# Kernel tuning notes

Measured on AMD Instinct MI355X. Metric: run time of the kernel, lower is better.

Reference implementation:

```python
import jax, jax.numpy as jnp
import numpy as np

B, P, ENC, DEC, ATT, EMB, V, MAXLEN = 64, 196, 2048, 1024, 1024, 1024, 10000, 20


def setup_inputs() -> dict:
    key = jax.random.key(0)
    ks = jax.random.split(key, 20)
    s = 0.02
    inp = {
        'encoder_out': jax.random.normal(ks[0], (B, 14, 14, ENC), jnp.float32),
        'encoded_captions': jax.random.randint(ks[1], (B, MAXLEN), 0, V),
        'caption_lengths': jax.random.randint(ks[2], (B, 1), 2, MAXLEN + 1).at[0, 0].set(MAXLEN),
        # embedding
        'emb_table': jax.random.uniform(ks[3], (V, EMB), jnp.float32, -0.1, 0.1),
        # attention MLP (weight_norm Linear == plain Linear math)
        'We': jax.random.normal(ks[4], (ATT, ENC)) * s,
        'be': jnp.zeros((ATT,), jnp.float32),
        'Wd': jax.random.normal(ks[5], (ATT, DEC)) * s,
        'bd': jnp.zeros((ATT,), jnp.float32),
        'Wf': jax.random.normal(ks[6], (1, ATT)) * s,
        'bf': jnp.zeros((1,), jnp.float32),
        # top_down_attention LSTMCell: input = EMB+ENC+DEC
        'W_ih1': jax.random.normal(ks[7], (4 * DEC, EMB + ENC + DEC)) * s,
        'W_hh1': jax.random.normal(ks[8], (4 * DEC, DEC)) * s,
        'b_ih1': jnp.zeros((4 * DEC,), jnp.float32),
        'b_hh1': jnp.zeros((4 * DEC,), jnp.float32),
        # language_model LSTMCell: input = ENC+DEC
        'W_ih2': jax.random.normal(ks[9], (4 * DEC, ENC + DEC)) * s,
        'W_hh2': jax.random.normal(ks[10], (4 * DEC, DEC)) * s,
        'b_ih2': jnp.zeros((4 * DEC,), jnp.float32),
        'b_hh2': jnp.zeros((4 * DEC,), jnp.float32),
        # output heads
        'Wfc1': jax.random.normal(ks[11], (V, DEC)) * s,
        'bfc1': jnp.zeros((V,), jnp.float32),
        'Wfc': jax.random.uniform(ks[12], (V, DEC), jnp.float32, -0.1, 0.1),
        'bfc': jnp.zeros((V,), jnp.float32),
    }
    return inp


def _lstm_cell(x, h, c, Wih, Whh, bih, bhh):
    g = x @ Wih.T + bih + h @ Whh.T + bhh
    i, f, gg, o = jnp.split(g, 4, axis=-1)  # torch gate order: i, f, g, o
    c2 = jax.nn.sigmoid(f) * c + jax.nn.sigmoid(i) * jnp.tanh(gg)
    h2 = jax.nn.sigmoid(o) * jnp.tanh(c2)
    return h2, c2


def _decode(encoder_out, encoded_captions, caption_lengths, emb_table,
            We, be, Wd, bd, Wf, bf,
            W_ih1, W_hh1, b_ih1, b_hh1, W_ih2, W_hh2, b_ih2, b_hh2,
            Wfc1, bfc1, Wfc, bfc):
    b = encoder_out.shape[0]
    enc = encoder_out.reshape(b, -1, encoder_out.shape[-1])  # (B,P,ENC)
    enc_mean = enc.mean(axis=1)
    cl = caption_lengths.squeeze(1)
    sort_ind = jnp.argsort(-cl)
    cl = cl[sort_ind]
    enc = enc[sort_ind]
    enc_mean = enc_mean[sort_ind]
    caps = encoded_captions[sort_ind]
    dec_len = cl - 1  # (B,)
    embeds = emb_table[caps]  # (B,T,EMB)
    Tdec = caps.shape[1] - 1
    # precompute encoder attention projection (loop-invariant, same math)
    att1 = jnp.einsum('bpe,ae->bpa', enc, We) + be  # (B,P,ATT)

    def step(carry, t):
        h1, c1, h2, c2 = carry
        active = (t < dec_len)[:, None]  # (B,1)
        x1 = jnp.concatenate([h2, enc_mean, embeds[:, t, :]], axis=1)
        h1n, c1n = _lstm_cell(x1, h1, c1, W_ih1, W_hh1, b_ih1, b_hh1)
        h1n = jnp.where(active, h1n, h1)
        c1n = jnp.where(active, c1n, c1)
        # Bahdanau attention
        att2 = h1n @ Wd.T + bd  # (B,ATT)
        e = jnp.einsum('bpa,a->bp', jax.nn.relu(att1 + att2[:, None, :]), Wf[0]) + bf[0]
        alpha = jax.nn.softmax(e, axis=1)
        awe = jnp.einsum('bpe,bp->be', enc, alpha)
        preds1 = h1n @ Wfc1.T + bfc1  # dropout is identity at eval
        x2 = jnp.concatenate([awe, h1n], axis=1)
        h2n, c2n = _lstm_cell(x2, h2, c2, W_ih2, W_hh2, b_ih2, b_hh2)
        h2n = jnp.where(active, h2n, h2)
        c2n = jnp.where(active, c2n, c2)
        preds = h2n @ Wfc.T + bfc
        preds = jnp.where(active, preds, 0.0)
        preds1 = jnp.where(active, preds1, 0.0)
        return (h1n, c1n, h2n, c2n), (preds, preds1)

    z = jnp.zeros((b, DEC), jnp.float32)
    (_, _, _, _), (pr, pr1) = jax.lax.scan(step, (z, z, z, z), jnp.arange(Tdec))
    predictions = jnp.transpose(pr, (1, 0, 2))  # (B,Tdec,V)
    predictions1 = jnp.transpose(pr1, (1, 0, 2))
    return predictions, predictions1, caps, dec_len, sort_ind


def reference(encoder_out, encoded_captions, caption_lengths, emb_table,
              We, be, Wd, bd, Wf, bf,
              W_ih1, W_hh1, b_ih1, b_hh1, W_ih2, W_hh2, b_ih2, b_hh2,
              Wfc1, bfc1, Wfc, bfc):
    return _decode(encoder_out, encoded_captions, caption_lengths, emb_table,
                   We, be, Wd, bd, Wf, bf,
                   W_ih1, W_hh1, b_ih1, b_hh1, W_ih2, W_hh2, b_ih2, b_hh2,
                   Wfc1, bfc1, Wfc, bfc)
```

## Files before the change

kernel.cpp:

```cpp
#include <hip/hip_runtime.h>
#include <cmath>

#define B_ 64
#define P_ 196
#define ENC_ 2048
#define DEC_ 1024
#define V_ 10000
#define MAXLEN_ 20
#define TDEC_ 19

typedef __attribute__((ext_vector_type(8))) short bf16x8;
typedef __attribute__((ext_vector_type(4))) float f32x4;


__device__ __align__(16) short g_encb[(size_t)12544 * 2048];
__device__ __align__(16) short g_encbt[(size_t)12544 * 2048];
__device__ __align__(16) short g_att1[(size_t)12544 * 1024];
__device__ __align__(16) short g_Wp1t[(size_t)4096 * 2048];
__device__ __align__(16) short g_Wmid1t[(size_t)4096 * 3072];
__device__ __align__(16) short g_Wc2t[(size_t)4096 * 4096];
__device__ __align__(16) short g_Webt[(size_t)1024 * 2048];
__device__ __align__(16) short g_Wdt[(size_t)1024 * 1024];
__device__ __align__(16) short g_Wfc1t[(size_t)10000 * 1024];
__device__ __align__(16) short g_Wfct[(size_t)10000 * 1024];
__device__ __align__(16) short g_xs1[(size_t)20 * 64 * 2048];
__device__ __align__(16) short g_xmid[(size_t)19 * 64 * 3072];
__device__ __align__(16) short g_xc2[(size_t)20 * 64 * 4096];
__device__ __align__(16) short g_em[64 * 2048];
__device__ __align__(16) float g_pre1[(size_t)19 * 64 * 4096];
__device__ __align__(16) float g_part[(size_t)8 * 64 * 4096];
__device__ __align__(16) float g_att2p[(size_t)4 * 64 * 1024];
__device__ __align__(16) float g_e[64 * P_];
__device__ __align__(16) float g_c1[64 * 1024];
__device__ __align__(16) float g_c2[64 * 1024];
__device__ int g_ibuf[64 + 64 + 64 * MAXLEN_];

__device__ __forceinline__ short f2b(float f) {
  unsigned u = __float_as_uint(f);
  u += 0x7FFFu + ((u >> 16) & 1u);
  return (short)(u >> 16);
}
__device__ __forceinline__ float b2f(short s) {
  return __uint_as_float(((unsigned)(unsigned short)s) << 16);
}

__global__ void k_sort(const int* __restrict__ cl_in, const int* __restrict__ caps_in,
                       int* __restrict__ sind, int* __restrict__ declen, int* __restrict__ caps_s,
                       float* __restrict__ out_caps, float* __restrict__ out_declen,
                       float* __restrict__ out_sind) {
  int i = threadIdx.x;
  __shared__ int cl[B_];
  cl[i] = cl_in[i];
  __syncthreads();
  int my = cl[i], pos = 0;
  for (int j = 0; j < B_; ++j) {
    int cj = cl[j];
    if (cj > my || (cj == my && j < i)) pos++;
  }
  sind[pos] = i;
  __syncthreads();
  int sb = sind[i];
  int dl = cl[sb] - 1;
  declen[i] = dl;
  out_declen[i] = (float)dl;
  out_sind[i] = (float)sb;
  for (int t = 0; t < MAXLEN_; ++t) {
    int v = caps_in[sb * MAXLEN_ + t];
    caps_s[i * MAXLEN_ + t] = v;
    out_caps[i * MAXLEN_ + t] = (float)v;
  }
}

__global__ __launch_bounds__(256) void k_encprep(const float* __restrict__ enc,
                                                 const int* __restrict__ sind,
                                                 short* __restrict__ encb,
                                                 short* __restrict__ encbt) {
  int mg = blockIdx.x;
  int b = mg / P_, p = mg - b * P_;
  int tid = threadIdx.x;
  const float* src = enc + ((size_t)sind[b] * P_ + p) * ENC_ + tid * 8;
  float4 a = *(const float4*)src;
  float4 c = *(const float4*)(src + 4);
  bf16x8 v;
  v[0] = f2b(a.x); v[1] = f2b(a.y); v[2] = f2b(a.z); v[3] = f2b(a.w);
  v[4] = f2b(c.x); v[5] = f2b(c.y); v[6] = f2b(c.z); v[7] = f2b(c.w);
  *(bf16x8*)(encb + (size_t)mg * ENC_ + tid * 8) = v;
  size_t off = (((size_t)(mg >> 4) * 64 + (tid >> 2)) << 9) +
               (((mg & 15) | ((tid & 3) << 4)) << 3);
  *(bf16x8*)(encbt + off) = v;
}

__global__ __launch_bounds__(256) void k_encmeanb(const short* __restrict__ encb,
                                                  short* __restrict__ em) {
  int b = blockIdx.x;
  int col0 = threadIdx.x * 8;
  const short* src = encb + (size_t)b * P_ * ENC_ + col0;
  float acc[8] = {};
  for (int p = 0; p < P_; ++p) {
    bf16x8 v = *(const bf16x8*)(src + (size_t)p * ENC_);
#pragma unroll
    for (int j = 0; j < 8; ++j) acc[j] += b2f(v[j]);
  }
#pragma unroll
  for (int j = 0; j < 8; ++j) em[b * 2048 + col0 + j] = f2b(acc[j] * (1.0f / 196.0f));
}

__global__ __launch_bounds__(256) void k_prefill(const float* __restrict__ emb,
                                                 const int* __restrict__ caps_s,
                                                 const short* __restrict__ em,
                                                 short* __restrict__ xmid) {
  int t = blockIdx.x, b = blockIdx.y, tid = threadIdx.x;
  short* xr = xmid + ((size_t)t * 64 + b) * 3072;
  int i = tid * 8;
  *(bf16x8*)(xr + i) = *(const bf16x8*)(em + b * 2048 + i);
  int cap = caps_s[b * MAXLEN_ + t];
  int j = tid * 4;
  float4 v = *(const float4*)(emb + (size_t)cap * 1024 + j);
  short4 o;
  o.x = f2b(v.x); o.y = f2b(v.y); o.z = f2b(v.z); o.w = f2b(v.w);
  *(short4*)(xr + 2048 + j) = o;
}

__global__ void k_f2bts(const float* __restrict__ src, int Kstride, int c0, int ncols,
                        short* __restrict__ dst, int Ktot, int koff) {
  int idx = blockIdx.x * 256 + threadIdx.x;
  int kc = ncols >> 3;
  int r = idx / kc, k8 = (idx - r * kc) << 3;
  const float* s = src + (size_t)r * Kstride + c0 + k8;
  float4 a = *(const float4*)s;
  float4 c = *(const float4*)(s + 4);
  bf16x8 v;
  v[0] = f2b(a.x); v[1] = f2b(a.y); v[2] = f2b(a.z); v[3] = f2b(a.w);
  v[4] = f2b(c.x); v[5] = f2b(c.y); v[6] = f2b(c.z); v[7] = f2b(c.w);
  int kg = koff + k8;
  size_t off = (((size_t)(r >> 4) * (Ktot >> 5) + (kg >> 5)) << 9) +
               (((r & 15) | (((kg >> 3) & 3) << 4)) << 3);
  *(bf16x8*)(dst + off) = v;
}

__global__ __launch_bounds__(1024) void k_att1_t(const short* __restrict__ At,
                                                 const short* __restrict__ Wt,
                                                 const float* __restrict__ be,
                                                 short* __restrict__ Cb) {
  int wave = threadIdx.x >> 6, lane = threadIdx.x & 63;
  int mt0 = blockIdx.x * 8 + (wave >> 3) * 4;
  int nt0 = blockIdx.y * 32 + (wave & 7) * 4;
  f32x4 acc[4][4] = {};
  const short* Ab = At + ((size_t)mt0 * 64 << 9) + lane * 8;
  const short* Wb = Wt + ((size_t)nt0 * 64 << 9) + lane * 8;
  for (int kt = 0; kt < 64; ++kt) {
    bf16x8 a[4], b[4];
#pragma unroll
    for (int i = 0; i < 4; ++i) a[i] = *(const bf16x8*)(Ab + (((size_t)i * 64 + kt) << 9));
#pragma unroll
    for (int j = 0; j < 4; ++j) b[j] = *(const bf16x8*)(Wb + (((size_t)j * 64 + kt) << 9));
#pragma unroll
    for (int i = 0; i < 4; ++i)
#pragma unroll
      for (int j = 0; j < 4; ++j)
        acc[i][j] = __builtin_amdgcn_mfma_f32_16x16x32_bf16(a[i], b[j], acc[i][j], 0, 0, 0);
  }
  int rr = (lane >> 4) * 4, cc = lane & 15;
  int m0 = mt0 * 16, n0 = nt0 * 16;
#pragma unroll
  for (int i = 0; i < 4; ++i)
#pragma unroll
    for (int j = 0; j < 4; ++j) {
      int n = n0 + j * 16 + cc;
      float bn = be[n];
#pragma unroll
      for (int r = 0; r < 4; ++r) {
        int m = m0 + i * 16 + rr + r;
        Cb[(size_t)m * 1024 + n] = f2b(acc[i][j][r] + bn);
      }
    }
}

__global__ __launch_bounds__(256) void k_skinny_t(const short* __restrict__ A, int lda,
                                                  const short* __restrict__ Wt, int ldw,
                                                  int N, int kchunk, float* __restrict__ part) {
  int wave = threadIdx.x >> 6, lane = threadIdx.x & 63;
  int n0 = blockIdx.x * 128 + wave * 32;
  int kb = blockIdx.y * kchunk;
  int lr = lane & 15, lk = (lane >> 4) * 8;
  int ntk = ldw >> 5;
  int nt0 = n0 >> 4;
  f32x4 acc[4][2] = {};
  const short* Ab = A + (size_t)lr * lda + kb + lk;
  const short* Wb0 = Wt + (((size_t)nt0 * ntk + (kb >> 5)) << 9) + lane * 8;
  const short* Wb1 = Wt + (((size_t)(nt0 + 1) * ntk + (kb >> 5)) << 9) + lane * 8;
  int nkt = kchunk >> 5;
  for (int kt = 0; kt < nkt; ++kt) {
    bf16x8 a[4], b0, b1;
#pragma unroll
    for (int i = 0; i < 4; ++i) a[i] = *(const bf16x8*)(Ab + (size_t)i * 16 * lda + kt * 32);
    b0 = *(const bf16x8*)(Wb0 + ((size_t)kt << 9));
    b1 = *(const bf16x8*)(Wb1 + ((size_t)kt << 9));
#pragma unroll
    for (int i = 0; i < 4; ++i) {
      acc[i][0] = __builtin_amdgcn_mfma_f32_16x16x32_bf16(a[i], b0, acc[i][0], 0, 0, 0);
      acc[i][1] = __builtin_amdgcn_mfma_f32_16x16x32_bf16(a[i], b1, acc[i][1], 0, 0, 0);
    }
  }
  float* po = part + (size_t)blockIdx.y * 64 * N;
  int rr = (lane >> 4) * 4, cc = lane & 15;
#pragma unroll
  for (int i = 0; i < 4; ++i)
#pragma unroll
    for (int j = 0; j < 2; ++j) {
      int n = n0 + j * 16 + cc;
#pragma unroll
      for (int r = 0; r < 4; ++r) {
        int m = i * 16 + rr + r;
        po[(size_t)m * N + n] = acc[i][j][r];
      }
    }
}

__global__ __launch_bounds__(256) void k_mid_bt(const short* __restrict__ xmid,
                                                const short* __restrict__ Wt,
                                                float* __restrict__ pre1) {
  int t = blockIdx.y;
  const short* A = xmid + (size_t)t * 64 * 3072;
  int wave = threadIdx.x >> 6, lane = threadIdx.x & 63;
  int n0 = blockIdx.x * 128 + wave * 32;
  int lr = lane & 15, lk = (lane >> 4) * 8;
  int nt0 = n0 >> 4;
  f32x4 acc[4][2] = {};
  const short* Ab = A + (size_t)lr * 3072 + lk;
  const short* Wb0 = Wt + (((size_t)nt0 * 96) << 9) + lane * 8;
  const short* Wb1 = Wt + (((size_t)(nt0 + 1) * 96) << 9) + lane * 8;
  for (int kt = 0; kt < 96; ++kt) {
    bf16x8 a[4], b0, b1;
#pragma unroll
    for (int i = 0; i < 4; ++i) a[i] = *(const bf16x8*)(Ab + (size_t)i * 16 * 3072 + kt * 32);
    b0 = *(const bf16x8*)(Wb0 + ((size_t)kt << 9));
    b1 = *(const bf16x8*)(Wb1 + ((size_t)kt << 9));
#pragma unroll
    for (int i = 0; i < 4; ++i) {
      acc[i][0] = __builtin_amdgcn_mfma_f32_16x16x32_bf16(a[i], b0, acc[i][0], 0, 0, 0);
      acc[i][1] = __builtin_amdgcn_mfma_f32_16x16x32_bf16(a[i], b1, acc[i][1], 0, 0, 0);
    }
  }
  float* po = pre1 + (size_t)t * 64 * 4096;
  int rr = (lane >> 4) * 4, cc = lane & 15;
#pragma unroll
  for (int i = 0; i < 4; ++i)
#pragma unroll
    for (int j = 0; j < 2; ++j) {
      int n = n0 + j * 16 + cc;
#pragma unroll
      for (int r = 0; r < 4; ++r) {
        int m = i * 16 + rr + r;
        po[(size_t)m * 4096 + n] = acc[i][j][r];
      }
    }
}

__global__ void k_gates(const float* __restrict__ part, int nsplit,
                        const float* __restrict__ pre,
                        const float* __restrict__ bih, const float* __restrict__ bhh,
                        float* __restrict__ c,
                        const short* __restrict__ hold, int ldo,
                        short* __restrict__ dst1, int ld1,
                        short* __restrict__ dst2, int ld2,
                        const int* __restrict__ declen, int t) {
  int idx = blockIdx.x * 256 + threadIdx.x;
  int b = idx >> 10, j = idx & 1023;
  const float* pb = part + (size_t)b * 4096;
  float gi = bih[j] + bhh[j];
  float gf = bih[1024 + j] + bhh[1024 + j];
  float gg = bih[2048 + j] + bhh[2048 + j];
  float go = bih[3072 + j] + bhh[3072 + j];
  if (pre) {
    const float* pp = pre + (size_t)b * 4096;
    gi += pp[j]; gf += pp[j + 1024]; gg += pp[j + 2048]; go += pp[j + 3072];
  }
  for (int s = 0; s < nsplit; ++s) {
    const float* p = pb + (size_t)s * 64 * 4096;
    gi += p[j]; gf += p[j + 1024]; gg += p[j + 2048]; go += p[j + 3072];
  }
  float si = 1.0f / (1.0f + expf(-gi));
  float sf = 1.0f / (1.0f + expf(-gf));
  float so = 1.0f / (1.0f + expf(-go));
  float cn = sf * c[idx] + si * tanhf(gg);
  float hn = so * tanhf(cn);
  short hb;
  if (t < declen[b]) {
    c[idx] = cn;
    hb = f2b(hn);
  } else {
    hb = hold[b * ldo + j];
  }
  dst1[b * ld1 + j] = hb;
  dst2[b * ld2 + j] = hb;
}

__global__ __launch_bounds__(256) void k_e(const short* __restrict__ att1,
                                           const float* __restrict__ att2p,
                                           const float* __restrict__ bd,
                                           const float* __restrict__ Wf,
                                           const float* __restrict__ bf,
                                           float* __restrict__ e) {
  __shared__ float a2[1024];
  int b = blockIdx.x / 49, pq = blockIdx.x % 49;
  for (int i = threadIdx.x; i < 1024; i += 256) {
    float s = bd[i];
#pragma unroll
    for (int q = 0; q < 4; ++q) s += att2p[q * 65536 + b * 1024 + i];
    a2[i] = s;
  }
  __syncthreads();
  int wave = threadIdx.x >> 6, lane = threadIdx.x & 63;
  int p = pq * 4 + wave;
  const short* a1 = att1 + ((size_t)(b * P_ + p)) * 1024;
  float s = 0.0f;
#pragma unroll
  for (int h = 0; h < 2; ++h) {
    int k0 = lane * 8 + h * 512;
    bf16x8 v = *(const bf16x8*)(a1 + k0);
#pragma unroll
    for (int j = 0; j < 8; ++j) s += Wf[k0 + j] * fmaxf(b2f(v[j]) + a2[k0 + j], 0.0f);
  }
#pragma unroll
  for (int off = 32; off; off >>= 1) s += __shfl_down(s, off);
  if (lane == 0) e[b * P_ + p] = s + bf[0];
}

__global__ __launch_bounds__(256) void k_sawe(const float* __restrict__ e,
                                              const short* __restrict__ encb,
                                              short* __restrict__ xc2t) {
  int b = blockIdx.x, ch = blockIdx.y;
  __shared__ float al[P_];
  __shared__ float red[8][256];
  int tid = threadIdx.x;
  if (tid < 64) {
    float vals[4];
    float mx = -1e30f;
#pragma unroll
    for (int q = 0; q < 4; ++q) {
      int p = tid + q * 64;
      vals[q] = (p < P_) ? e[b * P_ + p] : -1e30f;
      mx = fmaxf(mx, vals[q]);
    }
#pragma unroll
    for (int off = 32; off; off >>= 1) mx = fmaxf(mx, __shfl_xor(mx, off));
    float sum = 0.0f;
#pragma unroll
    for (int q = 0; q < 4; ++q) {
      int p = tid + q * 64;
      vals[q] = (p < P_) ? expf(vals[q] - mx) : 0.0f;
      sum += vals[q];
    }
#pragma unroll
    for (int off = 32; off; off >>= 1) sum += __shfl_xor(sum, off);
    float inv = 1.0f / sum;
#pragma unroll
    for (int q = 0; q < 4; ++q) {
      int p = tid + q * 64;
      if (p < P_) al[p] = vals[q] * inv;
    }
  }
  __syncthreads();
  int pg = tid >> 5, cg = tid & 31;
  int col = ch * 256 + cg * 8;
  const short* src = encb + (size_t)b * P_ * ENC_ + col;
  float acc[8] = {};
  for (int p = pg; p < P_; p += 8) {
    bf16x8 v = *(const bf16x8*)(src + (size_t)p * ENC_);
    float ap = al[p];
#pragma unroll
    for (int j = 0; j < 8; ++j) acc[j] += ap * b2f(v[j]);
  }
#pragma unroll
  for (int j = 0; j < 8; ++j) red[pg][cg * 8 + j] = acc[j];
  __syncthreads();
  float s = 0.0f;
#pragma unroll
  for (int g = 0; g < 8; ++g) s += red[g][tid];
  xc2t[b * 4096 + ch * 256 + tid] = f2b(s);
}

__global__ __launch_bounds__(256) void k_head4(const short* __restrict__ Aall,
                                               const short* __restrict__ Wt,
                                               const float* __restrict__ bias,
                                               float* __restrict__ outp,
                                               const int* __restrict__ declen) {
  int t = blockIdx.y;
  const short* A = Aall + (size_t)t * (64 * 4096);
  int wave = threadIdx.x >> 6, lane = threadIdx.x & 63;
  int nt0 = blockIdx.x * 16 + wave * 4;
  int lr = lane & 15, lk = (lane >> 4) * 8;
  f32x4 acc[4][4] = {};
  const short* Ab = A + (size_t)lr * 4096 + lk;
  const short* Wb[4];
  bool ok[4];
#pragma unroll
  for (int j = 0; j < 4; ++j) {
    ok[j] = (nt0 + j) < (V_ >> 4);
    Wb[j] = Wt + ((size_t)(ok[j] ? nt0 + j : 0) * 32 << 9) + lane * 8;
  }
  for (int kt = 0; kt < 32; ++kt) {
    bf16x8 a[4], b[4];
#pragma unroll
    for (int j = 0; j < 4; ++j) b[j] = *(const bf16x8*)(Wb[j] + ((size_t)kt << 9));
#pragma unroll
    for (int i = 0; i < 4; ++i) a[i] = *(const bf16x8*)(Ab + (size_t)i * 16 * 4096 + kt * 32);
#pragma unroll
    for (int i = 0; i < 4; ++i)
#pragma unroll
      for (int j = 0; j < 4; ++j)
        acc[i][j] = __builtin_amdgcn_mfma_f32_16x16x32_bf16(a[i], b[j], acc[i][j], 0, 0, 0);
  }
  int rr = (lane >> 4) * 4, cc = lane & 15;
#pragma unroll
  for (int j = 0; j < 4; ++j) {
    if (!ok[j]) continue;
    int n = (nt0 + j) * 16 + cc;
    float bn = bias[n];
#pragma unroll
    for (int i = 0; i < 4; ++i) {
#pragma unroll
      for (int r = 0; r < 4; ++r) {
        int b = i * 16 + rr + r;
        float val = acc[i][j][r] + bn;
        outp[((size_t)b * TDEC_ + t) * V_ + n] = (t < declen[b]) ? val : 0.0f;
      }
    }
  }
}

extern "C" void kernel_launch(void* const* d_in, const int* in_sizes, int n_in,
                              void* d_out, int out_size, void* d_ws, size_t ws_size,
                              hipStream_t stream) {
  (void)in_sizes; (void)n_in; (void)d_ws; (void)ws_size; (void)out_size;
  const float* enc  = (const float*)d_in[0];
  const int*   caps = (const int*)d_in[1];
  const int*   cl   = (const int*)d_in[2];
  const float* emb  = (const float*)d_in[3];
  const float* We   = (const float*)d_in[4];
  const float* be   = (const float*)d_in[5];
  const float* Wd   = (const float*)d_in[6];
  const float* bd   = (const float*)d_in[7];
  const float* Wf   = (const float*)d_in[8];
  const float* bf   = (const float*)d_in[9];
  const float* Wih1 = (const float*)d_in[10];
  const float* Whh1 = (const float*)d_in[11];
  const float* bih1 = (const float*)d_in[12];
  const float* bhh1 = (const float*)d_in[13];
  const float* Wih2 = (const float*)d_in[14];
  const float* Whh2 = (const float*)d_in[15];
  const float* bih2 = (const float*)d_in[16];
  const float* bhh2 = (const float*)d_in[17];
  const float* Wfc1 = (const float*)d_in[18];
  const float* bfc1 = (const float*)d_in[19];
  const float* Wfc  = (const float*)d_in[20];
  const float* bfc  = (const float*)d_in[21];
  float* out = (float*)d_out;

  short *encb, *encbt, *att1, *Wp1t, *Wmid1t, *Wc2t, *Webt, *Wdt, *Wfc1t, *Wfct;
  short *xs1, *xmid, *xc2, *em;
  float *pre1, *part, *att2p, *e, *c1, *c2;
  int* ib;
  hipGetSymbolAddress((void**)&encb, HIP_SYMBOL(g_encb));
  hipGetSymbolAddress((void**)&encbt, HIP_SYMBOL(g_encbt));
  hipGetSymbolAddress((void**)&att1, HIP_SYMBOL(g_att1));
  hipGetSymbolAddress((void**)&Wp1t, HIP_SYMBOL(g_Wp1t));
  hipGetSymbolAddress((void**)&Wmid1t, HIP_SYMBOL(g_Wmid1t));
  hipGetSymbolAddress((void**)&Wc2t, HIP_SYMBOL(g_Wc2t));
  hipGetSymbolAddress((void**)&Webt, HIP_SYMBOL(g_Webt));
  hipGetSymbolAddress((void**)&Wdt, HIP_SYMBOL(g_Wdt));
  hipGetSymbolAddress((void**)&Wfc1t, HIP_SYMBOL(g_Wfc1t));
  hipGetSymbolAddress((void**)&Wfct, HIP_SYMBOL(g_Wfct));
  hipGetSymbolAddress((void**)&xs1, HIP_SYMBOL(g_xs1));
  hipGetSymbolAddress((void**)&xmid, HIP_SYMBOL(g_xmid));
  hipGetSymbolAddress((void**)&xc2, HIP_SYMBOL(g_xc2));
  hipGetSymbolAddress((void**)&em, HIP_SYMBOL(g_em));
  hipGetSymbolAddress((void**)&pre1, HIP_SYMBOL(g_pre1));
  hipGetSymbolAddress((void**)&part, HIP_SYMBOL(g_part));
  hipGetSymbolAddress((void**)&att2p, HIP_SYMBOL(g_att2p));
  hipGetSymbolAddress((void**)&e, HIP_SYMBOL(g_e));
  hipGetSymbolAddress((void**)&c1, HIP_SYMBOL(g_c1));
  hipGetSymbolAddress((void**)&c2, HIP_SYMBOL(g_c2));
  hipGetSymbolAddress((void**)&ib, HIP_SYMBOL(g_ibuf));
  int* sind = ib;
  int* declen = ib + 64;
  int* caps_s = ib + 128;

  float* out_preds  = out;
  float* out_preds1 = out + (size_t)B_ * TDEC_ * V_;
  float* out_caps   = out + 2ull * B_ * TDEC_ * V_;
  float* out_declen = out_caps + B_ * MAXLEN_;
  float* out_sind   = out_declen + B_;

  k_sort<<<1, 64, 0, stream>>>(cl, caps, sind, declen, caps_s, out_caps, out_declen, out_sind);
  hipMemsetAsync(c1, 0, 64 * 1024 * sizeof(float), stream);
  hipMemsetAsync(c2, 0, 64 * 1024 * sizeof(float), stream);
  hipMemsetAsync(xs1, 0, (size_t)64 * 2048 * sizeof(short), stream);
  hipMemsetAsync(xc2, 0, (size_t)64 * 4096 * sizeof(short), stream);
  k_encprep<<<12544, 256, 0, stream>>>(enc, sind, encb, encbt);
  k_encmeanb<<<64, 256, 0, stream>>>(encb, em);
  k_prefill<<<dim3(19, 64), 256, 0, stream>>>(emb, caps_s, em, xmid);
  k_f2bts<<<2048, 256, 0, stream>>>(Wih1, 4096, 0, 1024, Wp1t, 2048, 0);
  k_f2bts<<<2048, 256, 0, stream>>>(Whh1, 1024, 0, 1024, Wp1t, 2048, 1024);
  k_f2bts<<<6144, 256, 0, stream>>>(Wih1, 4096, 1024, 3072, Wmid1t, 3072, 0);
  k_f2bts<<<6144, 256, 0, stream>>>(Wih2, 3072, 0, 3072, Wc2t, 4096, 0);
  k_f2bts<<<2048, 256, 0, stream>>>(Whh2, 1024, 0, 1024, Wc2t, 4096, 3072);
  k_f2bts<<<1024, 256, 0, stream>>>(We, 2048, 0, 2048, Webt, 2048, 0);
  k_f2bts<<<512, 256, 0, stream>>>(Wd, 1024, 0, 1024, Wdt, 1024, 0);
  k_f2bts<<<5000, 256, 0, stream>>>(Wfc1, 1024, 0, 1024, Wfc1t, 1024, 0);
  k_f2bts<<<5000, 256, 0, stream>>>(Wfc, 1024, 0, 1024, Wfct, 1024, 0);
  k_att1_t<<<dim3(98, 2), 1024, 0, stream>>>(encbt, Webt, be, att1);
  k_mid_bt<<<dim3(32, 19), 256, 0, stream>>>(xmid, Wmid1t, pre1);

  for (int t = 0; t < TDEC_; ++t) {
    short* s1t = xs1 + (size_t)t * 64 * 2048;
    short* s1n = xs1 + (size_t)(t + 1) * 64 * 2048;
    short* x2t = xc2 + (size_t)t * 64 * 4096;
    short* x2n = xc2 + (size_t)(t + 1) * 64 * 4096;
    k_skinny_t<<<dim3(32, 8), 256, 0, stream>>>(s1t, 2048, Wp1t, 2048, 4096, 256, part);
    k_gates<<<256, 256, 0, stream>>>(part, 8, pre1 + (size_t)t * 64 * 4096,
                                     bih1, bhh1, c1, s1t + 1024, 2048,
                                     s1n + 1024, 2048, x2t + 2048, 4096, declen, t);
    k_skinny_t<<<dim3(8, 4), 256, 0, stream>>>(x2t + 2048, 4096, Wdt, 1024, 1024, 256, att2p);
    k_e<<<3136, 256, 0, stream>>>(att1, att2p, bd, Wf, bf, e);
    k_sawe<<<dim3(64, 8), 256, 0, stream>>>(e, encb, x2t);
    k_skinny_t<<<dim3(32, 8), 256, 0, stream>>>(x2t, 4096, Wc2t, 4096, 4096, 512, part);
    k_gates<<<256, 256, 0, stream>>>(part, 8, nullptr, bih2, bhh2, c2, s1t, 2048,
                                     s1n, 2048, x2n + 3072, 4096, declen, t);
  }
  k_head4<<<dim3(40, 19), 256, 0, stream>>>(xc2 + 2048, Wfc1t, bfc1, out_preds1, declen);
  k_head4<<<dim3(40, 19), 256, 0, stream>>>(xc2 + 64 * 4096 + 3072, Wfct, bfc, out_preds, declen);
}
```

Measured before the change: 1.944 ms.

## Hoist time-invariant mean-encoder projection out of per-step LSTM1 input GEMM

```diff
diff --git a/kernel.cpp b/kernel.cpp
--- a/kernel.cpp
+++ b/kernel.cpp
@@ -17,17 +17,19 @@
 __device__ __align__(16) short g_encbt[(size_t)12544 * 2048];
 __device__ __align__(16) short g_att1[(size_t)12544 * 1024];
 __device__ __align__(16) short g_Wp1t[(size_t)4096 * 2048];
-__device__ __align__(16) short g_Wmid1t[(size_t)4096 * 3072];
+__device__ __align__(16) short g_Wemt[(size_t)4096 * 2048];
+__device__ __align__(16) short g_Wembt[(size_t)4096 * 1024];
 __device__ __align__(16) short g_Wc2t[(size_t)4096 * 4096];
 __device__ __align__(16) short g_Webt[(size_t)1024 * 2048];
 __device__ __align__(16) short g_Wdt[(size_t)1024 * 1024];
 __device__ __align__(16) short g_Wfc1t[(size_t)10000 * 1024];
 __device__ __align__(16) short g_Wfct[(size_t)10000 * 1024];
 __device__ __align__(16) short g_xs1[(size_t)20 * 64 * 2048];
-__device__ __align__(16) short g_xmid[(size_t)19 * 64 * 3072];
+__device__ __align__(16) short g_xemb[(size_t)19 * 64 * 1024];
 __device__ __align__(16) short g_xc2[(size_t)20 * 64 * 4096];
 __device__ __align__(16) short g_em[64 * 2048];
-__device__ __align__(16) float g_pre1[(size_t)19 * 64 * 4096];
+__device__ __align__(16) float g_preemb[(size_t)19 * 64 * 4096];
+__device__ __align__(16) float g_preem[64 * 4096];
 __device__ __align__(16) float g_part[(size_t)8 * 64 * 4096];
 __device__ __align__(16) float g_att2p[(size_t)4 * 64 * 1024];
 __device__ __align__(16) float g_e[64 * P_];
@@ -107,18 +109,15 @@
 
 __global__ __launch_bounds__(256) void k_prefill(const float* __restrict__ emb,
                                                  const int* __restrict__ caps_s,
-                                                 const short* __restrict__ em,
-                                                 short* __restrict__ xmid) {
+                                                 short* __restrict__ xemb) {
   int t = blockIdx.x, b = blockIdx.y, tid = threadIdx.x;
-  short* xr = xmid + ((size_t)t * 64 + b) * 3072;
-  int i = tid * 8;
-  *(bf16x8*)(xr + i) = *(const bf16x8*)(em + b * 2048 + i);
+  short* xr = xemb + ((size_t)t * 64 + b) * 1024;
   int cap = caps_s[b * MAXLEN_ + t];
   int j = tid * 4;
   float4 v = *(const float4*)(emb + (size_t)cap * 1024 + j);
   short4 o;
   o.x = f2b(v.x); o.y = f2b(v.y); o.z = f2b(v.z); o.w = f2b(v.w);
-  *(short4*)(xr + 2048 + j) = o;
+  *(short4*)(xr + j) = o;
 }
 
 __global__ void k_f2bts(const float* __restrict__ src, int Kstride, int c0, int ncols,
@@ -217,38 +216,45 @@
     }
 }
 
-__global__ __launch_bounds__(256) void k_mid_bt(const short* __restrict__ xmid,
-                                                const short* __restrict__ Wt,
-                                                float* __restrict__ pre1) {
-  int t = blockIdx.y;
-  const short* A = xmid + (size_t)t * 64 * 3072;
+__global__ void k_sumn(const float* __restrict__ part, int nsplit, float* __restrict__ dst) {
+  int idx = blockIdx.x * 256 + threadIdx.x;
+  float s = 0.0f;
+  for (int q = 0; q < nsplit; ++q) s += part[(size_t)q * 64 * 4096 + idx];
+  dst[idx] = s;
+}
+
+__global__ __launch_bounds__(256) void k_mid_emb4(const short* __restrict__ xemb,
+                                                  const short* __restrict__ Wt,
+                                                  float* __restrict__ preemb) {
+  int t = blockIdx.x;
+  const short* A = xemb + (size_t)t * 64 * 1024;
   int wave = threadIdx.x >> 6, lane = threadIdx.x & 63;
-  int n0 = blockIdx.x * 128 + wave * 32;
+  int nt0 = blockIdx.y * 16 + wave * 4;
   int lr = lane & 15, lk = (lane >> 4) * 8;
-  int nt0 = n0 >> 4;
-  f32x4 acc[4][2] = {};
-  const short* Ab = A + (size_t)lr * 3072 + lk;
-  const short* Wb0 = Wt + (((size_t)nt0 * 96) << 9) + lane * 8;
-  const short* Wb1 = Wt + (((size_t)(nt0 + 1) * 96) << 9) + lane * 8;
-  for (int kt = 0; kt < 96; ++kt) {
-    bf16x8 a[4], b0, b1;
-#pragma unroll
-    for (int i = 0; i < 4; ++i) a[i] = *(const bf16x8*)(Ab + (size_t)i * 16 * 3072 + kt * 32);
-    b0 = *(const bf16x8*)(Wb0 + ((size_t)kt << 9));
-    b1 = *(const bf16x8*)(Wb1 + ((size_t)kt << 9));
-#pragma unroll
-    for (int i = 0; i < 4; ++i) {
-      acc[i][0] = __builtin_amdgcn_mfma_f32_16x16x32_bf16(a[i], b0, acc[i][0], 0, 0, 0);
-      acc[i][1] = __builtin_amdgcn_mfma_f32_16x16x32_bf16(a[i], b1, acc[i][1], 0, 0, 0);
-    }
-  }
-  float* po = pre1 + (size_t)t * 64 * 4096;
+  f32x4 acc[4][4] = {};
+  const short* Ab = A + (size_t)lr * 1024 + lk;
+  const short* Wb[4];
+#pragma unroll
+  for (int j = 0; j < 4; ++j) Wb[j] = Wt + ((size_t)(nt0 + j) * 32 << 9) + lane * 8;
+  for (int kt = 0; kt < 32; ++kt) {
+    bf16x8 a[4], b[4];
+#pragma unroll
+    for (int j = 0; j < 4; ++j) b[j] = *(const bf16x8*)(Wb[j] + ((size_t)kt << 9));
+#pragma unroll
+    for (int i = 0; i < 4; ++i) a[i] = *(const bf16x8*)(Ab + (size_t)i * 16 * 1024 + kt * 32);
+#pragma unroll
+    for (int i = 0; i < 4; ++i)
+#pragma unroll
+      for (int j = 0; j < 4; ++j)
+        acc[i][j] = __builtin_amdgcn_mfma_f32_16x16x32_bf16(a[i], b[j], acc[i][j], 0, 0, 0);
+  }
+  float* po = preemb + (size_t)t * 64 * 4096;
   int rr = (lane >> 4) * 4, cc = lane & 15;
 #pragma unroll
   for (int i = 0; i < 4; ++i)
 #pragma unroll
-    for (int j = 0; j < 2; ++j) {
-      int n = n0 + j * 16 + cc;
+    for (int j = 0; j < 4; ++j) {
+      int n = (nt0 + j) * 16 + cc;
 #pragma unroll
       for (int r = 0; r < 4; ++r) {
         int m = i * 16 + rr + r;
@@ -258,7 +264,7 @@
 }
 
 __global__ void k_gates(const float* __restrict__ part, int nsplit,
-                        const float* __restrict__ pre,
+                        const float* __restrict__ pre, const float* __restrict__ pre2,
                         const float* __restrict__ bih, const float* __restrict__ bhh,
                         float* __restrict__ c,
                         const short* __restrict__ hold, int ldo,
@@ -276,6 +282,10 @@
     const float* pp = pre + (size_t)b * 4096;
     gi += pp[j]; gf += pp[j + 1024]; gg += pp[j + 2048]; go += pp[j + 3072];
   }
+  if (pre2) {
+    const float* pp = pre2 + (size_t)b * 4096;
+    gi += pp[j]; gf += pp[j + 1024]; gg += pp[j + 2048]; go += pp[j + 3072];
+  }
   for (int s = 0; s < nsplit; ++s) {
     const float* p = pb + (size_t)s * 64 * 4096;
     gi += p[j]; gf += p[j + 1024]; gg += p[j + 2048]; go += p[j + 3072];
@@ -386,10 +396,10 @@
                                                const float* __restrict__ bias,
                                                float* __restrict__ outp,
                                                const int* __restrict__ declen) {
-  int t = blockIdx.y;
+  int t = blockIdx.x;
   const short* A = Aall + (size_t)t * (64 * 4096);
   int wave = threadIdx.x >> 6, lane = threadIdx.x & 63;
-  int nt0 = blockIdx.x * 16 + wave * 4;
+  int nt0 = blockIdx.y * 16 + wave * 4;
   int lr = lane & 15, lk = (lane >> 4) * 8;
   f32x4 acc[4][4] = {};
   const short* Ab = A + (size_t)lr * 4096 + lk;
@@ -458,25 +468,27 @@
   const float* bfc  = (const float*)d_in[21];
   float* out = (float*)d_out;
 
-  short *encb, *encbt, *att1, *Wp1t, *Wmid1t, *Wc2t, *Webt, *Wdt, *Wfc1t, *Wfct;
-  short *xs1, *xmid, *xc2, *em;
-  float *pre1, *part, *att2p, *e, *c1, *c2;
+  short *encb, *encbt, *att1, *Wp1t, *Wemt, *Wembt, *Wc2t, *Webt, *Wdt, *Wfc1t, *Wfct;
+  short *xs1, *xemb, *xc2, *em;
+  float *preemb, *preem, *part, *att2p, *e, *c1, *c2;
   int* ib;
   hipGetSymbolAddress((void**)&encb, HIP_SYMBOL(g_encb));
   hipGetSymbolAddress((void**)&encbt, HIP_SYMBOL(g_encbt));
   hipGetSymbolAddress((void**)&att1, HIP_SYMBOL(g_att1));
   hipGetSymbolAddress((void**)&Wp1t, HIP_SYMBOL(g_Wp1t));
-  hipGetSymbolAddress((void**)&Wmid1t, HIP_SYMBOL(g_Wmid1t));
+  hipGetSymbolAddress((void**)&Wemt, HIP_SYMBOL(g_Wemt));
+  hipGetSymbolAddress((void**)&Wembt, HIP_SYMBOL(g_Wembt));
   hipGetSymbolAddress((void**)&Wc2t, HIP_SYMBOL(g_Wc2t));
   hipGetSymbolAddress((void**)&Webt, HIP_SYMBOL(g_Webt));
   hipGetSymbolAddress((void**)&Wdt, HIP_SYMBOL(g_Wdt));
   hipGetSymbolAddress((void**)&Wfc1t, HIP_SYMBOL(g_Wfc1t));
   hipGetSymbolAddress((void**)&Wfct, HIP_SYMBOL(g_Wfct));
   hipGetSymbolAddress((void**)&xs1, HIP_SYMBOL(g_xs1));
-  hipGetSymbolAddress((void**)&xmid, HIP_SYMBOL(g_xmid));
+  hipGetSymbolAddress((void**)&xemb, HIP_SYMBOL(g_xemb));
   hipGetSymbolAddress((void**)&xc2, HIP_SYMBOL(g_xc2));
   hipGetSymbolAddress((void**)&em, HIP_SYMBOL(g_em));
-  hipGetSymbolAddress((void**)&pre1, HIP_SYMBOL(g_pre1));
+  hipGetSymbolAddress((void**)&preemb, HIP_SYMBOL(g_preemb));
+  hipGetSymbolAddress((void**)&preem, HIP_SYMBOL(g_preem));
   hipGetSymbolAddress((void**)&part, HIP_SYMBOL(g_part));
   hipGetSymbolAddress((void**)&att2p, HIP_SYMBOL(g_att2p));
   hipGetSymbolAddress((void**)&e, HIP_SYMBOL(g_e));
@@ -500,10 +512,11 @@
   hipMemsetAsync(xc2, 0, (size_t)64 * 4096 * sizeof(short), stream);
   k_encprep<<<12544, 256, 0, stream>>>(enc, sind, encb, encbt);
   k_encmeanb<<<64, 256, 0, stream>>>(encb, em);
-  k_prefill<<<dim3(19, 64), 256, 0, stream>>>(emb, caps_s, em, xmid);
+  k_prefill<<<dim3(19, 64), 256, 0, stream>>>(emb, caps_s, xemb);
   k_f2bts<<<2048, 256, 0, stream>>>(Wih1, 4096, 0, 1024, Wp1t, 2048, 0);
   k_f2bts<<<2048, 256, 0, stream>>>(Whh1, 1024, 0, 1024, Wp1t, 2048, 1024);
-  k_f2bts<<<6144, 256, 0, stream>>>(Wih1, 4096, 1024, 3072, Wmid1t, 3072, 0);
+  k_f2bts<<<4096, 256, 0, stream>>>(Wih1, 4096, 1024, 2048, Wemt, 2048, 0);
+  k_f2bts<<<2048, 256, 0, stream>>>(Wih1, 4096, 3072, 1024, Wembt, 1024, 0);
   k_f2bts<<<6144, 256, 0, stream>>>(Wih2, 3072, 0, 3072, Wc2t, 4096, 0);
   k_f2bts<<<2048, 256, 0, stream>>>(Whh2, 1024, 0, 1024, Wc2t, 4096, 3072);
   k_f2bts<<<1024, 256, 0, stream>>>(We, 2048, 0, 2048, Webt, 2048, 0);
@@ -511,7 +524,9 @@
   k_f2bts<<<5000, 256, 0, stream>>>(Wfc1, 1024, 0, 1024, Wfc1t, 1024, 0);
   k_f2bts<<<5000, 256, 0, stream>>>(Wfc, 1024, 0, 1024, Wfct, 1024, 0);
   k_att1_t<<<dim3(98, 2), 1024, 0, stream>>>(encbt, Webt, be, att1);
-  k_mid_bt<<<dim3(32, 19), 256, 0, stream>>>(xmid, Wmid1t, pre1);
+  k_skinny_t<<<dim3(32, 4), 256, 0, stream>>>(em, 2048, Wemt, 2048, 4096, 512, part);
+  k_sumn<<<1024, 256, 0, stream>>>(part, 4, preem);
+  k_mid_emb4<<<dim3(19, 16), 256, 0, stream>>>(xemb, Wembt, preemb);
 
   for (int t = 0; t < TDEC_; ++t) {
     short* s1t = xs1 + (size_t)t * 64 * 2048;
@@ -519,16 +534,16 @@
     short* x2t = xc2 + (size_t)t * 64 * 4096;
     short* x2n = xc2 + (size_t)(t + 1) * 64 * 4096;
     k_skinny_t<<<dim3(32, 8), 256, 0, stream>>>(s1t, 2048, Wp1t, 2048, 4096, 256, part);
-    k_gates<<<256, 256, 0, stream>>>(part, 8, pre1 + (size_t)t * 64 * 4096,
+    k_gates<<<256, 256, 0, stream>>>(part, 8, preemb + (size_t)t * 64 * 4096, preem,
                                      bih1, bhh1, c1, s1t + 1024, 2048,
                                      s1n + 1024, 2048, x2t + 2048, 4096, declen, t);
     k_skinny_t<<<dim3(8, 4), 256, 0, stream>>>(x2t + 2048, 4096, Wdt, 1024, 1024, 256, att2p);
     k_e<<<3136, 256, 0, stream>>>(att1, att2p, bd, Wf, bf, e);
     k_sawe<<<dim3(64, 8), 256, 0, stream>>>(e, encb, x2t);
     k_skinny_t<<<dim3(32, 8), 256, 0, stream>>>(x2t, 4096, Wc2t, 4096, 4096, 512, part);
-    k_gates<<<256, 256, 0, stream>>>(part, 8, nullptr, bih2, bhh2, c2, s1t, 2048,
+    k_gates<<<256, 256, 0, stream>>>(part, 8, nullptr, nullptr, bih2, bhh2, c2, s1t, 2048,
                                      s1n, 2048, x2n + 3072, 4096, declen, t);
   }
-  k_head4<<<dim3(40, 19), 256, 0, stream>>>(xc2 + 2048, Wfc1t, bfc1, out_preds1, declen);
-  k_head4<<<dim3(40, 19), 256, 0, stream>>>(xc2 + 64 * 4096 + 3072, Wfct, bfc, out_preds, declen);
-}
+  k_head4<<<dim3(19, 40), 256, 0, stream>>>(xc2 + 2048, Wfc1t, bfc1, out_preds1, declen);
+  k_head4<<<dim3(19, 40), 256, 0, stream>>>(xc2 + 64 * 4096 + 3072, Wfct, bfc, out_preds, declen);
+}
```

New measurement: 1.865 ms. 1.04x faster.
